# Optimization experiments

Hardware: AMD Instinct MI355X
Metric: run time of the kernel (lower is better)

## Reference

```python
import jax, jax.numpy as jnp
import numpy as np

DIM = 512; NB = 4; BS = DIM // NB            # EinFFT blocks
DS = 64; DC = 4; EXP = 2; DI = EXP * DIM      # Mamba dims
DTR = DIM // 16                               # dt_rank
BLOCKS = 2; LAM = 0.01; B_SZ = 2; L_SZ = 1024

def layer_norm(x, w, b):
    m = x.mean(-1, keepdims=True)
    v = x.var(-1, keepdims=True)
    return (x - m) / jnp.sqrt(v + 1e-5) * w + b

def softshrink(x, lam):
    return jnp.where(x > lam, x - lam, jnp.where(x < -lam, x + lam, jnp.zeros((), x.dtype)))

def mamba(x, in_proj_w, conv_w, conv_b, x_proj_w, dt_proj_w, dt_proj_b, A_log, D, out_proj_w):
    B, L, _ = x.shape
    xz = x @ in_proj_w.T                      # (B,L,2*DI)
    xm, z = jnp.split(xz, 2, axis=-1)
    # causal depthwise conv1d, keep first L outputs
    xt = xm.transpose(0, 2, 1)                # (B,DI,L)
    conv = jax.lax.conv_general_dilated(xt, conv_w, (1,), [(DC - 1, 0)],
                                        feature_group_count=DI,
                                        dimension_numbers=('NCH', 'OIH', 'NCH'))
    xm = jax.nn.silu((conv + conv_b[None, :, None]).transpose(0, 2, 1))  # (B,L,DI)
    proj = xm @ x_proj_w.T                    # (B,L,DTR+2*DS)
    dt = proj[..., :DTR]
    Bm = proj[..., DTR:DTR + DS]
    Cm = proj[..., DTR + DS:]
    dt = jax.nn.softplus(dt @ dt_proj_w.T + dt_proj_b)   # (B,L,DI)
    A = -jnp.exp(A_log)                       # (DI,DS)

    def step(h, inp):
        dt_t, B_t, C_t, u_t = inp             # (B,DI),(B,DS),(B,DS),(B,DI)
        dA = jnp.exp(dt_t[:, :, None] * A)
        h = dA * h + dt_t[:, :, None] * B_t[:, None, :] * u_t[:, :, None]
        y = jnp.einsum('bds,bs->bd', h, C_t)
        return h, y

    h0 = jnp.zeros((B, DI, DS), x.dtype)
    _, ys = jax.lax.scan(step, h0, (dt.transpose(1, 0, 2), Bm.transpose(1, 0, 2),
                                    Cm.transpose(1, 0, 2), xm.transpose(1, 0, 2)))
    y = ys.transpose(1, 0, 2) + xm * D        # (B,L,DI)
    y = y * jax.nn.silu(z)
    return y @ out_proj_w.T

def einfft(x, cw1, cw2, cb1, cb2):
    B, N, C = x.shape
    xf = jnp.fft.fft2(x.reshape(B, N, NB, BS), axes=(1, 2), norm='ortho')
    mul = lambda t, w: jnp.einsum('BNbd,bdk->BNbk', t, w)
    r1 = jax.nn.relu(mul(xf.real, cw1[0]) - mul(xf.imag, cw1[1]) + cb1[0])
    i1 = jax.nn.relu(mul(xf.real, cw1[1]) + mul(xf.imag, cw1[0]) + cb1[1])
    r2 = softshrink(mul(r1, cw2[0]) - mul(i1, cw2[1]) + cb2[0], LAM)
    i2 = softshrink(mul(r1, cw2[1]) + mul(i1, cw2[0]) + cb2[1], LAM)
    out = jnp.fft.ifft2(r2 + 1j * i2, axes=(1, 2), norm='ortho')
    return out.real.astype(x.dtype).reshape(B, N, C)

def setup_inputs() -> dict:
    key = jax.random.key(0)
    ks = jax.random.split(key, 16)
    r = lambda i, shape, s: jax.random.normal(ks[i], shape, jnp.float32) * s
    A_log = jnp.log(jnp.tile(jnp.arange(1, DS + 1, dtype=jnp.float32), (DI, 1)))
    return {
        'x': jax.random.normal(ks[0], (B_SZ, L_SZ, DIM), jnp.float32),
        'ln_w': jnp.ones((DIM,), jnp.float32), 'ln_b': jnp.zeros((DIM,), jnp.float32),
        'in_proj_w': r(1, (2 * DI, DIM), 0.02),
        'conv_w': r(2, (DI, 1, DC), 0.1), 'conv_b': jnp.zeros((DI,), jnp.float32),
        'x_proj_w': r(3, (DTR + 2 * DS, DI), 0.02),
        'dt_proj_w': r(4, (DI, DTR), 0.02),
        'dt_proj_b': jnp.full((DI,), float(np.log(np.expm1(0.01))), jnp.float32),
        'A_log': A_log, 'D': jnp.ones((DI,), jnp.float32),
        'out_proj_w': r(5, (DIM, DI), 0.02),
        'norm2_w': jnp.ones((DIM,), jnp.float32), 'norm2_b': jnp.zeros((DIM,), jnp.float32),
        'cw1': r(6, (2, NB, BS, BS), 0.02), 'cw2': r(7, (2, NB, BS, BS), 0.02),
        'cb1': r(8, (2, NB, BS), 0.02), 'cb2': r(9, (2, NB, BS), 0.02),
    }

def reference(x, ln_w, ln_b, in_proj_w, conv_w, conv_b, x_proj_w, dt_proj_w, dt_proj_b,
              A_log, D, out_proj_w, norm2_w, norm2_b, cw1, cw2, cb1, cb2):
    for _ in range(BLOCKS):
        x = x + mamba(layer_norm(x, ln_w, ln_b), in_proj_w, conv_w, conv_b,
                      x_proj_w, dt_proj_w, dt_proj_b, A_log, D, out_proj_w)
        x = x + einfft(layer_norm(x, norm2_w, norm2_b), cw1, cw2, cb1, cb2)
    return x
```

## Files before the change

### kernel.cpp

```cpp
#include <hip/hip_runtime.h>

typedef unsigned short u16;
typedef __attribute__((ext_vector_type(8))) short bf8;
typedef __attribute__((ext_vector_type(4))) float f4;

__device__ __forceinline__ float bf2f(u16 b) {
    return __uint_as_float(((unsigned)b) << 16);
}
__device__ __forceinline__ u16 f2bf(float f) {
    unsigned u = __float_as_uint(f);
    u += 0x7fffu + ((u >> 16) & 1u);
    return (u16)(u >> 16);
}
__device__ __forceinline__ void pack8f(const float* v, u16* dst) {
    uint r0 = (uint)f2bf(v[0]) | ((uint)f2bf(v[1]) << 16);
    uint r1 = (uint)f2bf(v[2]) | ((uint)f2bf(v[3]) << 16);
    uint r2 = (uint)f2bf(v[4]) | ((uint)f2bf(v[5]) << 16);
    uint r3 = (uint)f2bf(v[6]) | ((uint)f2bf(v[7]) << 16);
    *(uint4*)dst = make_uint4(r0, r1, r2, r3);
}
__device__ __forceinline__ bf8 neg8(bf8 v) {
    union { bf8 b; uint u[4]; } t; t.b = v;
    t.u[0] ^= 0x80008000u; t.u[1] ^= 0x80008000u;
    t.u[2] ^= 0x80008000u; t.u[3] ^= 0x80008000u;
// ... 21 lines not shown

struct CvtArgs {
    const void* src[18];
    void* dst[18];
    int n[18];
    int obf[18];
};
__global__ __launch_bounds__(256)
void cvt_all_k(CvtArgs a, const int* __restrict__ flag) {
    const int t = blockIdx.y;
    const int n = a.n[t];
    const int f = flag[0];
    if (a.obf[t] == 2) {
        u16* __restrict__ d = (u16*)a.dst[t];
        if (f) {
            const u16* __restrict__ s = (const u16*)a.src[t];
            for (int i = blockIdx.x * 256 + threadIdx.x; i < n; i += gridDim.x * 256) {
                int cin = i & 127, cout = (i >> 7) & 127, snb = i >> 14;
                d[(snb << 14) + (cout << 7) + cin] = s[(snb << 14) + (cin << 7) + cout];
            }
        } else {
            const float* __restrict__ s = (const float*)a.src[t];
            for (int i = blockIdx.x * 256 + threadIdx.x; i < n; i += gridDim.x * 256) {
                int cin = i & 127, cout = (i >> 7) & 127, snb = i >> 14;
                d[(snb << 14) + (cout << 7) + cin] =
                    f2bf(s[(snb << 14) + (cin << 7) + cout]);
            }
        }
    } else if (a.obf[t] == 1) {
        u16* __restrict__ d = (u16*)a.dst[t];
        if (f) {
            const u16* __restrict__ s = (const u16*)a.src[t];
            for (int i = blockIdx.x * 256 + threadIdx.x; i < n; i += gridDim.x * 256)
                d[i] = s[i];
        } else {
            const float* __restrict__ s = (const float*)a.src[t];
            for (int i = blockIdx.x * 256 + threadIdx.x; i < n; i += gridDim.x * 256)
                d[i] = f2bf(s[i]);
        }
    } else {
        float* __restrict__ d = (float*)a.dst[t];
        if (f) {
            const u16* __restrict__ s = (const u16*)a.src[t];
            for (int i = blockIdx.x * 256 + threadIdx.x; i < n; i += gridDim.x * 256)
                d[i] = bf2f(s[i]);
        } else {
            const float* __restrict__ s = (const float*)a.src[t];
            for (int i = blockIdx.x * 256 + threadIdx.x; i < n; i += gridDim.x * 256)
                d[i] = s[i];
        }
    }
}

__global__ void out_k(const float* __restrict__ in, void* __restrict__ out,
                      int n, const int* __restrict__ flag) {
    int i = blockIdx.x * 256 + threadIdx.x;
    if (i >= n) return;
    if (flag[0]) ((u16*)out)[i] = f2bf(in[i]);
    else         ((float*)out)[i] = in[i];
}

__global__ __launch_bounds__(256)
void ln_k(const float* __restrict__ x, const float* __restrict__ w,
          const float* __restrict__ b, u16* __restrict__ out) {
    const int row = blockIdx.x, tid = threadIdx.x;
    const float* xr = x + (long)row * 512;
    float v0 = xr[tid], v1 = xr[tid + 256];
    float s = v0 + v1, q = v0 * v0 + v1 * v1;
#pragma unroll
    for (int off = 32; off; off >>= 1) {
        s += __shfl_xor(s, off);
        q += __shfl_xor(q, off);
    }
    __shared__ float ss[4], qq[4];
    int wid = tid >> 6;
    if ((tid & 63) == 0) { ss[wid] = s; qq[wid] = q; }
    __syncthreads();
    s = ss[0] + ss[1] + ss[2] + ss[3];
    q = qq[0] + qq[1] + qq[2] + qq[3];
    float mean = s * (1.f / 512.f);
    float var = q * (1.f / 512.f) - mean * mean;
    float rstd = rsqrtf(var + 1e-5f);
    u16* o = out + (long)row * 512;
    o[tid]       = f2bf((v0 - mean) * rstd * w[tid]       + b[tid]);
    o[tid + 256] = f2bf((v1 - mean) * rstd * w[tid + 256] + b[tid + 256]);
}

#define LSTR 40
template <int TAF, int EPI>
__global__ __launch_bounds__(256)
void mgemm_k(const void* __restrict__ Ap, const u16* __restrict__ Bp,
             float* __restrict__ D, int N, int K, int lda, int ldb, int ldc,
             long bsA, long bsB, long bsC,
             const float* __restrict__ bias, const float* __restrict__ res) {
    const float* Af = (const float*)Ap + blockIdx.z * bsA;
    const u16*  Ab  = (const u16*)Ap + blockIdx.z * bsA;
    const u16*  B   = Bp + blockIdx.z * bsB;
    D += blockIdx.z * bsC;

    __shared__ u16 As[64 * LSTR];
    __shared__ u16 Bs[64 * LSTR];
    const int tid = threadIdx.x;
    const int lane = tid & 63;
    const int w = tid >> 6, wm = w & 1, wn = w >> 1;
    const int m0 = blockIdx.y * 64, n0 = blockIdx.x * 64;
    const int fr = (lane & 15), fq = (lane >> 4);

    f4 acc[2][2] = {};

    for (int k0 = 0; k0 < K; k0 += 32) {
        {
            const int ar = tid >> 2, aks = (tid & 3) << 3;
            if constexpr (TAF == 1) {
                *(uint4*)&As[ar * LSTR + aks] =
                    *(const uint4*)(Ab + (long)(m0 + ar) * lda + k0 + aks);
            } else if constexpr (TAF == 2) {
                const float* p = Af + (long)(m0 + ar) * lda + k0 + aks;
                float4 x = *(const float4*)p, y = *(const float4*)(p + 4);
#pragma unroll
                for (int pt = 1; pt < 4; ++pt) {
                    const float* pp = p + (long)pt * bsA;
                    float4 x1 = *(const float4*)pp, y1 = *(const float4*)(pp + 4);
                    x.x += x1.x; x.y += x1.y; x.z += x1.z; x.w += x1.w;
                    y.x += y1.x; y.y += y1.y; y.z += y1.z; y.w += y1.w;
                }
                float tv[8];
                tv[0] = x.x; tv[1] = x.y; tv[2] = x.z; tv[3] = x.w;
                tv[4] = y.x; tv[5] = y.y; tv[6] = y.z; tv[7] = y.w;
                pack8f(tv, &As[ar * LSTR + aks]);
            } else {
                const float* p = Af + (long)(m0 + ar) * lda + k0 + aks;
                float tv[8];
                float4 x = *(const float4*)p, y = *(const float4*)(p + 4);
                tv[0] = x.x; tv[1] = x.y; tv[2] = x.z; tv[3] = x.w;
                tv[4] = y.x; tv[5] = y.y; tv[6] = y.z; tv[7] = y.w;
                pack8f(tv, &As[ar * LSTR + aks]);
            }
        }
        {
            const int br = tid >> 2, bks = (tid & 3) << 3;
            uint4 raw = make_uint4(0, 0, 0, 0);
            if (n0 + br < N)
                raw = *(const uint4*)(B + (long)(n0 + br) * ldb + k0 + bks);
            *(uint4*)&Bs[br * LSTR + bks] = raw;
        }
        __syncthreads();
        bf8 af[2], bff[2];
#pragma unroll
        for (int t = 0; t < 2; t++) {
            af[t]  = *(bf8*)&As[(wm * 32 + t * 16 + fr) * LSTR + (fq << 3)];
            bff[t] = *(bf8*)&Bs[(wn * 32 + t * 16 + fr) * LSTR + (fq << 3)];
        }
#pragma unroll
        for (int i = 0; i < 2; i++)
#pragma unroll
            for (int j = 0; j < 2; j++)
                acc[i][j] = __builtin_amdgcn_mfma_f32_16x16x32_bf16(
                    af[i], bff[j], acc[i][j], 0, 0, 0);
        __syncthreads();
    }

#pragma unroll
    for (int i = 0; i < 2; i++) {
#pragma unroll
        for (int j = 0; j < 2; j++) {
            const int gmb = m0 + wm * 32 + i * 16 + (fq << 2);
            const int gn  = n0 + wn * 32 + j * 16 + fr;
            if (gn >= N) continue;
            float v[4];
#pragma unroll
            for (int e = 0; e < 4; e++) v[e] = acc[i][j][e];
            if constexpr (EPI == 1 || EPI == 3) {
                float bb = bias[gn];
#pragma unroll
                for (int e = 0; e < 4; e++) {
                    float t = v[e] + bb;
                    v[e] = (t > 20.f) ? t : log1pf(__expf(t));
                }
            }
#pragma unroll
            for (int e = 0; e < 4; e++) {
                long idx = (long)(gmb + e) * ldc + gn;
                float t = v[e];
                if constexpr (EPI == 2) t += res[idx];
                if constexpr (EPI == 3) ((u16*)D)[idx] = f2bf(t);
                else                    D[idx] = t;
            }
        }
    }
}

__global__ __launch_bounds__(256)
void gemm128_k(const u16* __restrict__ A, const u16* __restrict__ B,
               float* __restrict__ Dm, u16* __restrict__ Dz,
               int K, int lda, int ldb) {
    __shared__ u16 As[128 * LSTR];
    __shared__ u16 Bs[128 * LSTR];
    const int tid = threadIdx.x, lane = tid & 63;
    const int w = tid >> 6, wm = w & 1, wn = w >> 1;
    const int m0 = blockIdx.y * 128, n0 = blockIdx.x * 128;
    const int fr = lane & 15, fq = lane >> 4;
    f4 acc[4][4] = {};

    for (int k0 = 0; k0 < K; k0 += 32) {
#pragma unroll
        for (int j = 0; j < 2; ++j) {
            int idx = tid + j * 256;
            int row = idx >> 2, col = (idx & 3) << 3;
            *(uint4*)&As[row * LSTR + col] =
                *(const uint4*)(A + (long)(m0 + row) * lda + k0 + col);
            *(uint4*)&Bs[row * LSTR + col] =
                *(const uint4*)(B + (long)(n0 + row) * ldb + k0 + col);
        }
        __syncthreads();
        bf8 af[4], bfv[4];
#pragma unroll
        for (int i = 0; i < 4; ++i) {
            af[i]  = *(bf8*)&As[(wm * 64 + i * 16 + fr) * LSTR + (fq << 3)];
            bfv[i] = *(bf8*)&Bs[(wn * 64 + i * 16 + fr) * LSTR + (fq << 3)];
        }
#pragma unroll
        for (int i = 0; i < 4; ++i)
#pragma unroll
            for (int j = 0; j < 4; ++j)
                acc[i][j] = __builtin_amdgcn_mfma_f32_16x16x32_bf16(
                    af[i], bfv[j], acc[i][j], 0, 0, 0);
        __syncthreads();
    }
#pragma unroll
    for (int i = 0; i < 4; ++i)
#pragma unroll
        for (int j = 0; j < 4; ++j) {
            const int gm = m0 + wm * 64 + i * 16 + (fq << 2);
            const int gn = n0 + wn * 64 + j * 16 + fr;
            if (n0 < 1024) {
#pragma unroll
                for (int e = 0; e < 4; ++e)
                    Dm[(long)(gm + e) * 1024 + gn] = acc[i][j][e];
            } else {
#pragma unroll
                for (int e = 0; e < 4; ++e)
                    Dz[(long)(gm + e) * 1024 + (gn - 1024)] = f2bf(acc[i][j][e]);
            }
        }
}

__global__ __launch_bounds__(1024)
void ffw_k(const u16* __restrict__ xn, u16* __restrict__ Orb,
           u16* __restrict__ Oib) {
    const int bz = blockIdx.x;
    const int b = bz >> 7, cg = bz & 127;
    const int t = threadIdx.x;
    const int f = t >> 8, tl = t & 255;
    const int c = cg + f * 128;
    __shared__ float re[4224], im[4224], twr[768], twi[768];
    if (t < 768) {
        float s, cc;
        __sincosf((float)t * -6.1359231515425649e-3f, &s, &cc);
        twr[t] = cc; twi[t] = s;
    }
    float* rf = re + f * 1056;
    float* mf = im + f * 1056;
    const u16* src = xn + ((long)b * 1024) * 512 + c;
#pragma unroll
    for (int r = 0; r < 4; ++r) {
        int n = tl + r * 256;
        float v = bf2f(src[(long)n * 512]);
        int a = n + (n >> 5);
        rf[a] = v; mf[a] = 0.f;
    }
    __syncthreads();
#pragma unroll
    for (int st = 0; st < 5; ++st) {
        const int qsh = 8 - 2 * st;
        const int q = 1 << qsh;
        const int len = q << 2;
        const int m = 1 << (2 * st);
        int j = tl & (q - 1);
        int g = tl >> qsh;
        int i0 = g * len + j;
        int a0 = i0 + (i0 >> 5);
        int i1 = i0 + q,     a1 = i1 + (i1 >> 5);
        int i2 = i0 + 2 * q, a2 = i2 + (i2 >> 5);
        int i3 = i0 + 3 * q, a3 = i3 + (i3 >> 5);
        float ar = rf[a0], ai = mf[a0];
        float br = rf[a1], bi = mf[a1];
        float cr = rf[a2], ci = mf[a2];
        float dr = rf[a3], di = mf[a3];
        float t0r = ar + cr, t0i = ai + ci;
        float t1r = ar - cr, t1i = ai - ci;
        float t2r = br + dr, t2i = bi + di;
        float u = br - dr, v = bi - di;
        rf[a0] = t0r + t2r; mf[a0] = t0i + t2i;
        {
            int k = j * m;
            float wr = twr[k], wi = twi[k];
// ... 102 lines not shown
        const int q = 1 << qsh;
        const int len = q << 2;
        const int m = 1 << (2 * st);
        int j = tl & (q - 1);
        int g = tl >> qsh;
        int i0 = g * len + j;
        int a0 = i0 + (i0 >> 5);
        int i1 = i0 + q,     a1 = i1 + (i1 >> 5);
        int i2 = i0 + 2 * q, a2 = i2 + (i2 >> 5);
        int i3 = i0 + 3 * q, a3 = i3 + (i3 >> 5);
        float ar = rf[a0], ai = mf[a0];
        float br = rf[a1], bi = mf[a1];
        float cr = rf[a2], ci = mf[a2];
        float dr = rf[a3], di = mf[a3];
        float t0r = ar + cr, t0i = ai + ci;
        float t1r = ar - cr, t1i = ai - ci;
        float t2r = br + dr, t2i = bi + di;
        float u = br - dr, v = bi - di;
        rf[a0] = t0r + t2r; mf[a0] = t0i + t2i;
        {
            int k = j * m;
            float wr = twr[k], wi = twi[k];
            float xr = t1r - v, xi = t1i + u;
            rf[a1] = xr * wr - xi * wi;
            mf[a1] = xr * wi + xi * wr;
        }
        {
            int k = 2 * j * m;
            float wr = twr[k], wi = twi[k];
            float xr = t0r - t2r, xi = t0i - t2i;
            rf[a2] = xr * wr - xi * wi;
            mf[a2] = xr * wi + xi * wr;
        }
        {
            int k = 3 * j * m;
            float wr = twr[k], wi = twi[k];
            float xr = t1r + v, xi = t1i - u;
            rf[a3] = xr * wr - xi * wi;
            mf[a3] = xr * wi + xi * wr;
        }
        __syncthreads();
    }
    float* d = Yc + ((long)(b * 512 + c)) * 1024;
#pragma unroll
    for (int r = 0; r < 4; ++r) {
        int n = tl + r * 256;
        int sidx = digrev10(n);
        int a = sidx + (sidx >> 5);
        d[n] = rf[a] * 0.03125f;
    }
}

__global__ __launch_bounds__(256)
void transadd_k(float* __restrict__ xbuf, const float* __restrict__ Yc) {
    const int b = blockIdx.z;
    const int c0 = blockIdx.x * 64, n0 = blockIdx.y * 64;
    __shared__ float T[64][65];
    const int tid = threadIdx.x;
    const int r = tid >> 2, q = (tid & 3) * 16;
    const float* src = Yc + ((long)(b * 512 + c0 + r)) * 1024 + n0 + q;
#pragma unroll
    for (int k = 0; k < 4; ++k) {
        float4 v = *(const float4*)(src + k * 4);
        T[r][q + k * 4 + 0] = v.x; T[r][q + k * 4 + 1] = v.y;
        T[r][q + k * 4 + 2] = v.z; T[r][q + k * 4 + 3] = v.w;
    }
    __syncthreads();
    float* dst = xbuf + ((long)(b * 1024 + n0 + r)) * 512 + c0 + q;
#pragma unroll
    for (int k = 0; k < 4; ++k) {
        float4 w = *(const float4*)(dst + k * 4);
        w.x += T[q + k * 4 + 0][r]; w.y += T[q + k * 4 + 1][r];
        w.z += T[q + k * 4 + 2][r]; w.w += T[q + k * 4 + 3][r];
        *(float4*)(dst + k * 4) = w;
    }
}

#define LSTR2 136
template <int ACT>
__global__ __launch_bounds__(256)
void cmix_k(const u16* __restrict__ Xr, const u16* __restrict__ Xi,
            const u16* __restrict__ WT, const float* __restrict__ cb,
            u16* __restrict__ Or, u16* __restrict__ Oi) {
    const int z = blockIdx.z, b = z >> 2, nb = z & 3;
    const u16* Ar = Xr + (long)b * 524288 + nb * 131072;
    const u16* Ai = Xi + (long)b * 524288 + nb * 131072;
    const u16* Wr = WT + nb * 16384;
    const u16* Wi = WT + 65536 + nb * 16384;
    u16* Dr = Or + (long)b * 524288 + nb * 131072;
    u16* Di = Oi + (long)b * 524288 + nb * 131072;
    __shared__ u16 Ars[64 * LSTR2], Ais[64 * LSTR2], Brs[64 * LSTR2], Bis[64 * LSTR2];
    const int tid = threadIdx.x, lane = tid & 63;
    const int w = tid >> 6, wm = w & 1, wn = w >> 1;
    const int m0 = blockIdx.y * 64, n0 = blockIdx.x * 64;
    const int fr = (lane & 15), fq = (lane >> 4);
    f4 accr[2][2] = {}, acci[2][2] = {};

    {
        const int am = tid & 63, akb = (tid >> 6) << 3;
#pragma unroll
        for (int kk = 0; kk < 4; ++kk) {
            const int kb = kk * 32 + akb;
            u16 tr[8], ti[8];
#pragma unroll
            for (int j = 0; j < 8; j++) {
                long off = (long)(kb + j) * 1024 + m0 + am;
                tr[j] = Ar[off]; ti[j] = Ai[off];
            }
            uint r0 = (uint)tr[0] | ((uint)tr[1] << 16);
            uint r1 = (uint)tr[2] | ((uint)tr[3] << 16);
            uint r2 = (uint)tr[4] | ((uint)tr[5] << 16);
            uint r3 = (uint)tr[6] | ((uint)tr[7] << 16);
            *(uint4*)&Ars[am * LSTR2 + kb] = make_uint4(r0, r1, r2, r3);
            r0 = (uint)ti[0] | ((uint)ti[1] << 16);
            r1 = (uint)ti[2] | ((uint)ti[3] << 16);
            r2 = (uint)ti[4] | ((uint)ti[5] << 16);
            r3 = (uint)ti[6] | ((uint)ti[7] << 16);
            *(uint4*)&Ais[am * LSTR2 + kb] = make_uint4(r0, r1, r2, r3);
        }
        const int br = tid >> 2, bks = (tid & 3) << 3;
#pragma unroll
        for (int kk = 0; kk < 4; ++kk) {
            const int kb = kk * 32 + bks;
            *(uint4*)&Brs[br * LSTR2 + kb] =
                *(const uint4*)(Wr + (long)(n0 + br) * 128 + kb);
            *(uint4*)&Bis[br * LSTR2 + kb] =
                *(const uint4*)(Wi + (long)(n0 + br) * 128 + kb);
// ... 7 lines not shown
        bf8 arf[2], aif[2], brf[2], bif[2];
#pragma unroll
        for (int t = 0; t < 2; t++) {
            arf[t] = *(bf8*)&Ars[(wm * 32 + t * 16 + fr) * LSTR2 + kc];
            aif[t] = *(bf8*)&Ais[(wm * 32 + t * 16 + fr) * LSTR2 + kc];
            brf[t] = *(bf8*)&Brs[(wn * 32 + t * 16 + fr) * LSTR2 + kc];
            bif[t] = *(bf8*)&Bis[(wn * 32 + t * 16 + fr) * LSTR2 + kc];
        }
        bf8 nai[2] = { neg8(aif[0]), neg8(aif[1]) };
#pragma unroll
        for (int i = 0; i < 2; i++)
#pragma unroll
            for (int j = 0; j < 2; j++) {
                accr[i][j] = __builtin_amdgcn_mfma_f32_16x16x32_bf16(arf[i], brf[j], accr[i][j], 0, 0, 0);
                accr[i][j] = __builtin_amdgcn_mfma_f32_16x16x32_bf16(nai[i], bif[j], accr[i][j], 0, 0, 0);
                acci[i][j] = __builtin_amdgcn_mfma_f32_16x16x32_bf16(arf[i], bif[j], acci[i][j], 0, 0, 0);
                acci[i][j] = __builtin_amdgcn_mfma_f32_16x16x32_bf16(aif[i], brf[j], acci[i][j], 0, 0, 0);
            }
    }

#pragma unroll
    for (int i = 0; i < 2; i++)
#pragma unroll
        for (int j = 0; j < 2; j++) {
            const int gmb = m0 + wm * 32 + i * 16 + (fq << 2);
            const int gn  = n0 + wn * 32 + j * 16 + fr;
            const float bbr = cb[nb * 128 + gn];
            const float bbi = cb[512 + nb * 128 + gn];
            u16 pr[4], pi[4];
#pragma unroll
            for (int e = 0; e < 4; e++) {
                float vr = accr[i][j][e] + bbr;
                float vi = acci[i][j][e] + bbi;
                if (ACT == 0) {
                    vr = fmaxf(vr, 0.f);
                    vi = fmaxf(vi, 0.f);
                } else {
                    vr = (vr > 0.01f) ? vr - 0.01f : ((vr < -0.01f) ? vr + 0.01f : 0.f);
                    vi = (vi > 0.01f) ? vi - 0.01f : ((vi < -0.01f) ? vi + 0.01f : 0.f);
                }
                pr[e] = f2bf(vr); pi[e] = f2bf(vi);
            }
            uint2 wr2, wi2;
            wr2.x = (uint)pr[0] | ((uint)pr[1] << 16);
            wr2.y = (uint)pr[2] | ((uint)pr[3] << 16);
            wi2.x = (uint)pi[0] | ((uint)pi[1] << 16);
            wi2.y = (uint)pi[2] | ((uint)pi[3] << 16);
            *(uint2*)&Dr[(long)gn * 1024 + gmb] = wr2;
            *(uint2*)&Di[(long)gn * 1024 + gmb] = wi2;
        }
}

__global__ __launch_bounds__(256)
void conv_k(const float* __restrict__ xm, const float* __restrict__ cw,
            const float* __restrict__ cb, u16* __restrict__ u) {
    int idx = blockIdx.x * 256 + threadIdx.x;
    int d = idx & 1023;
    int l = (idx >> 10) & 1023;
    int b = idx >> 20;
    float acc = cb[d];
    const float* base = xm + (long)b * 1048576 + d;
#pragma unroll
    for (int j = 0; j < 4; j++) {
        int li = l - 3 + j;
        if (li >= 0) acc = fmaf(cw[d * 4 + j], base[(long)li * 1024], acc);
    }
    float sig = 1.f / (1.f + __expf(-acc));
    u[idx] = f2bf(acc * sig);
}

__global__ __launch_bounds__(256)
void scan1_k(const u16* __restrict__ dtb, const u16* __restrict__ uLb,
             const float* __restrict__ Pb, const float* __restrict__ alog,
             u16* __restrict__ Hb, float* __restrict__ Sbuf,
             float* __restrict__ Bred, float* __restrict__ Cred,
             const int* __restrict__ flag) {
    const int dg = blockIdx.x, c = blockIdx.y, b = blockIdx.z;
    const int tid = threadIdx.x;
    const int d = dg * 256 + tid;
    const int t0 = c * 16;
    __shared__ float Bls[16][64];
    {
        int r = tid >> 4, cg = (tid & 15) << 2;
        const float* src = Pb + ((long)(b * 1024 + t0 + r)) * 160 + 32 + cg;
        float4 v0 = *(const float4*)src;
        float4 v1 = *(const float4*)(src + 327680);
        float4 v2 = *(const float4*)(src + 655360);
        float4 v3 = *(const float4*)(src + 983040);
        v0.x += v1.x + v2.x + v3.x;
        v0.y += v1.y + v2.y + v3.y;
        v0.z += v1.z + v2.z + v3.z;
        v0.w += v1.w + v2.w + v3.w;
        *(float4*)&Bls[r][cg] = v0;
        if (dg == 0) {
            long ro = (((long)(b * 64 + c)) * 16 + r) * 64 + cg;
            *(float4*)&Bred[ro] = v0;
            float4 c0 = *(const float4*)(src + 64);
            float4 c1 = *(const float4*)(src + 64 + 327680);
            float4 c2 = *(const float4*)(src + 64 + 655360);
            float4 c3 = *(const float4*)(src + 64 + 983040);
            c0.x += c1.x + c2.x + c3.x;
            c0.y += c1.y + c2.y + c3.y;
            c0.z += c1.z + c2.z + c3.z;
            c0.w += c1.w + c2.w + c3.w;
            *(float4*)&Cred[ro] = c0;
        }
    }
    __syncthreads();

    float h[64];
#pragma unroll
    for (int s = 0; s < 64; s++) h[s] = 0.f;
    float S = 0.f;
    const u16* dtp = dtb + (long)(b * 1024 + t0) * 1024 + d;
    const u16* up  = uLb + (long)(b * 1024 + t0) * 1024 + d;

    if (flag[1]) {
        for (int t = 0; t < 16; ++t) {
            float dt = bf2f(dtp[(long)t * 1024]);
            float uu = bf2f(up[(long)t * 1024]);
            float dtu = dt * uu;
            S += dt;
            float q = __expf(-dt);
            float q2 = q * q, q3 = q2 * q, q4 = q2 * q2;
            float a0 = q, a1 = q2, a2 = q3, a3 = q4;
            const float4* B4p = (const float4*)&Bls[t][0];
#pragma unroll
            for (int sg = 0; sg < 16; ++sg) {
                float4 B4 = B4p[sg];
                h[sg * 4 + 0] = a0 * h[sg * 4 + 0] + dtu * B4.x;
                h[sg * 4 + 1] = a1 * h[sg * 4 + 1] + dtu * B4.y;
                h[sg * 4 + 2] = a2 * h[sg * 4 + 2] + dtu * B4.z;
                h[sg * 4 + 3] = a3 * h[sg * 4 + 3] + dtu * B4.w;
                a0 *= q4; a1 *= q4; a2 *= q4; a3 *= q4;
            }
        }
    } else {
        float A[64];
        const float* ap = alog + (long)d * 64;
#pragma unroll
        for (int s = 0; s < 64; s += 4) {
            float4 a4 = *(const float4*)(ap + s);
            A[s] = -__expf(a4.x); A[s + 1] = -__expf(a4.y);
            A[s + 2] = -__expf(a4.z); A[s + 3] = -__expf(a4.w);
        }
        for (int t = 0; t < 16; ++t) {
            float dt = bf2f(dtp[(long)t * 1024]);
            float uu = bf2f(up[(long)t * 1024]);
            float dtu = dt * uu;
            S += dt;
            const float4* B4p = (const float4*)&Bls[t][0];
#pragma unroll
            for (int sg = 0; sg < 16; ++sg) {
                float4 B4 = B4p[sg];
                h[sg * 4 + 0] = __expf(dt * A[sg * 4 + 0]) * h[sg * 4 + 0] + dtu * B4.x;
                h[sg * 4 + 1] = __expf(dt * A[sg * 4 + 1]) * h[sg * 4 + 1] + dtu * B4.y;
                h[sg * 4 + 2] = __expf(dt * A[sg * 4 + 2]) * h[sg * 4 + 2] + dtu * B4.z;
                h[sg * 4 + 3] = __expf(dt * A[sg * 4 + 3]) * h[sg * 4 + 3] + dtu * B4.w;
            }
        }
    }
    u16* Hp = Hb + ((((long)(b * 64 + c)) * 1024 + d) << 6);
#pragma unroll
    for (int s = 0; s < 64; s += 4) {
        uint2 p;
        p.x = ((__float_as_uint(h[s]) + 0x8000u) >> 16) |
              ((__float_as_uint(h[s + 1]) + 0x8000u) & 0xFFFF0000u);
        p.y = ((__float_as_uint(h[s + 2]) + 0x8000u) >> 16) |
              ((__float_as_uint(h[s + 3]) + 0x8000u) & 0xFFFF0000u);
        *(uint2*)&Hp[s] = p;
    }
    Sbuf[(b * 64 + c) * 1024 + d] = S;
}

__global__ __launch_bounds__(256)
void scan2_k(const float* __restrict__ alog, const float* __restrict__ Sbuf,
             u16* __restrict__ Hb) {
    int idx = blockIdx.x * 256 + threadIdx.x;
    int s = idx & 63, d = (idx >> 6) & 1023, b = idx >> 16;
    float A = -__expf(alog[(long)d * 64 + s]);
    float carry = 0.f;
    long off = ((((long)(b * 64)) * 1024 + d) << 6) + s;
    int sb = (b * 64) * 1024 + d;
    float Scur = Sbuf[sb];
    float Hcur = bf2f(Hb[off]);
    for (int c = 0; c < 64; ++c) {
        float Snxt = 0.f, Hnxt = 0.f;
        if (c < 63) {
            Snxt = Sbuf[sb + 1024];
            Hnxt = bf2f(Hb[off + 65536]);
        }
        float P = __expf(A * Scur);
        Hb[off] = (u16)((__float_as_uint(carry) + 0x8000u) >> 16);
        carry = P * carry + Hcur;
        Scur = Snxt; Hcur = Hnxt;
        off += 65536; sb += 1024;
    }
}

__global__ __launch_bounds__(256)
void scan3_k(const u16* __restrict__ dtb, const u16* __restrict__ uLb,
             const u16* __restrict__ zLb, const float* __restrict__ Bred,
             const float* __restrict__ Cred, const float* __restrict__ alog,
             const u16* __restrict__ Hb, const float* __restrict__ Dw,
             const int* __restrict__ flag, u16* __restrict__ y2) {
    const int dg = blockIdx.x, c = blockIdx.y, b = blockIdx.z;
    const int tid = threadIdx.x;
    const int d = dg * 256 + tid;
    const int t0 = c * 16;
    __shared__ float Bls[16][64];
    __shared__ float Cls[16][64];
    {
        int r = tid >> 4, cg = (tid & 15) << 2;
        long ro = (((long)(b * 64 + c)) * 16 + r) * 64 + cg;
        *(float4*)&Bls[r][cg] = *(const float4*)&Bred[ro];
        *(float4*)&Cls[r][cg] = *(const float4*)&Cred[ro];
    }
    __syncthreads();

    float h[64];
    const u16* Hp = Hb + ((((long)(b * 64 + c)) * 1024 + d) << 6);
#pragma unroll
    for (int s = 0; s < 64; s += 4) {
        uint2 p = *(const uint2*)&Hp[s];
        h[s]     = __uint_as_float(p.x << 16);
        h[s + 1] = __uint_as_float(p.x & 0xFFFF0000u);
        h[s + 2] = __uint_as_float(p.y << 16);
        h[s + 3] = __uint_as_float(p.y & 0xFFFF0000u);
    }
    const float Dd = Dw[d];
    const u16* dtp = dtb + (long)(b * 1024 + t0) * 1024 + d;
    const u16* up  = uLb + (long)(b * 1024 + t0) * 1024 + d;
    const u16* zp  = zLb + (long)(b * 1024 + t0) * 1024 + d;
    u16* y2p = y2 + (long)(b * 1024 + t0) * 1024 + d;

    if (flag[1]) {
        for (int t = 0; t < 16; ++t) {
            float dt = bf2f(dtp[(long)t * 1024]);
            float uu = bf2f(up[(long)t * 1024]);
            float zz = bf2f(zp[(long)t * 1024]);
            float dtu = dt * uu;
            float y = 0.f;
            float q = __expf(-dt);
            float q2 = q * q, q3 = q2 * q, q4 = q2 * q2;
            float a0 = q, a1 = q2, a2 = q3, a3 = q4;
            const float4* B4p = (const float4*)&Bls[t][0];
            const float4* C4p = (const float4*)&Cls[t][0];
#pragma unroll
            for (int sg = 0; sg < 16; ++sg) {
                float4 B4 = B4p[sg];
                float4 C4 = C4p[sg];
                h[sg * 4 + 0] = a0 * h[sg * 4 + 0] + dtu * B4.x;
                y = fmaf(h[sg * 4 + 0], C4.x, y);
                h[sg * 4 + 1] = a1 * h[sg * 4 + 1] + dtu * B4.y;
                y = fmaf(h[sg * 4 + 1], C4.y, y);
                h[sg * 4 + 2] = a2 * h[sg * 4 + 2] + dtu * B4.z;
                y = fmaf(h[sg * 4 + 2], C4.z, y);
                h[sg * 4 + 3] = a3 * h[sg * 4 + 3] + dtu * B4.w;
                y = fmaf(h[sg * 4 + 3], C4.w, y);
                a0 *= q4; a1 *= q4; a2 *= q4; a3 *= q4;
            }
            float g = zz / (1.f + __expf(-zz));
            y2p[(long)t * 1024] = f2bf((y + uu * Dd) * g);
        }
    } else {
        float A[64];
        const float* ap = alog + (long)d * 64;
#pragma unroll
        for (int s = 0; s < 64; s += 4) {
            float4 a4 = *(const float4*)(ap + s);
            A[s] = -__expf(a4.x); A[s + 1] = -__expf(a4.y);
            A[s + 2] = -__expf(a4.z); A[s + 3] = -__expf(a4.w);
        }
        for (int t = 0; t < 16; ++t) {
            float dt = bf2f(dtp[(long)t * 1024]);
            float uu = bf2f(up[(long)t * 1024]);
            float zz = bf2f(zp[(long)t * 1024]);
            float dtu = dt * uu;
            float y = 0.f;
            const float4* B4p = (const float4*)&Bls[t][0];
            const float4* C4p = (const float4*)&Cls[t][0];
#pragma unroll
            for (int sg = 0; sg < 16; ++sg) {
                float4 B4 = B4p[sg];
                float4 C4 = C4p[sg];
                h[sg * 4 + 0] = __expf(dt * A[sg * 4 + 0]) * h[sg * 4 + 0] + dtu * B4.x;
                y = fmaf(h[sg * 4 + 0], C4.x, y);
                h[sg * 4 + 1] = __expf(dt * A[sg * 4 + 1]) * h[sg * 4 + 1] + dtu * B4.y;
                y = fmaf(h[sg * 4 + 1], C4.y, y);
                h[sg * 4 + 2] = __expf(dt * A[sg * 4 + 2]) * h[sg * 4 + 2] + dtu * B4.z;
                y = fmaf(h[sg * 4 + 2], C4.z, y);
                h[sg * 4 + 3] = __expf(dt * A[sg * 4 + 3]) * h[sg * 4 + 3] + dtu * B4.w;
                y = fmaf(h[sg * 4 + 3], C4.w, y);
            }
            float g = zz / (1.f + __expf(-zz));
            y2p[(long)t * 1024] = f2bf((y + uu * Dd) * g);
        }
    }
}

extern "C" void kernel_launch(void* const* d_in, const int* in_sizes, int n_in,
                              void* d_out, int out_size, void* d_ws, size_t ws_size,
                              hipStream_t stream) {
    float* ws = (float*)d_ws;
    int* flag = (int*)ws;
    size_t o = 64;
    float* xbuf  = ws + o; o += 1048576;
    float* fftA  = ws + o; o += 3145728;
    float* xmL   = ws + o; o += 2097152;
    float* Yc    = ws + o; o += 1048576;
    u16* xnb     = (u16*)(ws + o); o += 524288;
    u16* wInpB   = (u16*)(ws + o); o += 524288;
    u16* wXpB    = (u16*)(ws + o); o += 81920;
    u16* wDtB    = (u16*)(ws + o); o += 16384;
    u16* wOutB   = (u16*)(ws + o); o += 262144;
    u16* WT1     = (u16*)(ws + o); o += 65536;
    u16* WT2     = (u16*)(ws + o); o += 65536;
    float* wConv = ws + o; o += 4096;
    float* wAlog = ws + o; o += 65536;
    float* wLnW  = ws + o; o += 512;
    float* wLnB  = ws + o; o += 512;
    float* wConvB= ws + o; o += 1024;
    float* wDtBias=ws + o; o += 1024;
    float* wD    = ws + o; o += 1024;
    float* wN2w  = ws + o; o += 512;
    float* wN2b  = ws + o; o += 512;
    float* wCb1  = ws + o; o += 1024;
    float* wCb2  = ws + o; o += 1024;
    float* Hreg  = ws + o; o += 4194304;
    float* Sbuf  = ws + o; o += 131072;
    float* Pbuf2 = ws + o; o += 1310720;
    u16* uLb     = (u16*)(ws + o); o += 1048576;
    u16* y2b     = (u16*)(ws + o); o += 524288;
    u16* dtLb    = (u16*)(ws + o); o += 1048576;
    u16* zLb     = (u16*)(ws + o); o += 1048576;
    float* Bred  = ws + o; o += 131072;
    float* Cred  = ws + o; o += 131072;
    u16* Hb    = (u16*)Hreg;
    u16* xzb  = (u16*)fftA;
    u16* Xrb  = xzb;
    u16* Xib  = xzb + 1048576;
    u16* r1b  = xzb + 2097152;
    u16* i1b  = xzb + 3145728;
    u16* X2rb = xzb + 4194304;
    u16* X2ib = xzb + 5242880;

    dim3 blk(256);

    detect_k<<<1, 1, 0, stream>>>((const u16*)d_in[8], flag);

    CvtArgs ca;
    void* dsts[18] = {xbuf, wLnW, wLnB, wInpB, wConv, wConvB, wXpB, wDtB, wDtBias,
                      wAlog, wD, wOutB, wN2w, wN2b, WT1, WT2, wCb1, wCb2};
    int obf[18]    = {0,    0,    0,    1,     0,     0,      1,    1,    0,
                      0,     0,  1,     0,    0,    2,   2,   0,    0};
    for (int i = 0; i < 18; i++) {
        ca.src[i] = d_in[i];
        ca.dst[i] = dsts[i];
        ca.n[i] = in_sizes[i];
        ca.obf[i] = obf[i];
    }
    cvt_all_k<<<dim3(64, 18), blk, 0, stream>>>(ca, flag);
    achk_k<<<256, blk, 0, stream>>>(wAlog, flag);

    for (int it = 0; it < 2; ++it) {
        ln_k<<<2048, blk, 0, stream>>>(xbuf, wLnW, wLnB, xnb);
        gemm128_k<<<dim3(16, 16), blk, 0, stream>>>(
            xnb, wInpB, xmL, zLb, 512, 512, 512);
        conv_k<<<8192, blk, 0, stream>>>(xmL, wConv, wConvB, uLb);
        mgemm_k<1, 0><<<dim3(3, 32, 4), blk, 0, stream>>>(
            uLb, wXpB, Pbuf2, 160, 256, 1024, 1024, 160,
            256, 256, 327680, nullptr, nullptr);
        mgemm_k<2, 3><<<dim3(16, 32, 1), blk, 0, stream>>>(
            Pbuf2, wDtB, (float*)dtLb, 1024, 32, 160, 32, 1024, 327680, 0, 0,
            wDtBias, nullptr);
        scan1_k<<<dim3(4, 64, 2), blk, 0, stream>>>(
            dtLb, uLb, Pbuf2, wAlog, Hb, Sbuf, Bred, Cred, flag);
        scan2_k<<<512, blk, 0, stream>>>(wAlog, Sbuf, Hb);
        scan3_k<<<dim3(4, 64, 2), blk, 0, stream>>>(
            dtLb, uLb, zLb, Bred, Cred, wAlog, Hb, wD, flag, y2b);
        mgemm_k<1, 2><<<dim3(8, 32, 1), blk, 0, stream>>>(
            y2b, wOutB, xbuf, 512, 1024, 1024, 1024, 512, 0, 0, 0, nullptr, xbuf);

        ln_k<<<2048, blk, 0, stream>>>(xbuf, wN2w, wN2b, xnb);
        ffw_k<<<256, dim3(1024), 0, stream>>>(xnb, Xrb, Xib);
        cmix_k<0><<<dim3(2, 16, 8), blk, 0, stream>>>(Xrb, Xib, WT1, wCb1, r1b, i1b);
        cmix_k<1><<<dim3(2, 16, 8), blk, 0, stream>>>(r1b, i1b, WT2, wCb2, X2rb, X2ib);
        ifw_k<<<256, dim3(1024), 0, stream>>>(X2rb, X2ib, Yc);
        transadd_k<<<dim3(8, 16, 2), blk, 0, stream>>>(xbuf, Yc);
    }

    out_k<<<(out_size + 255) / 256, blk, 0, stream>>>(xbuf, d_out, out_size, flag);
}
```

Measured before the change: 461.6 us.

## Fuse dt projection into scan1, enlarge scan chunks, store xm as bf16

The dt_proj GEMM with softplus is folded into scan1_k, which now computes dt per channel from shared-memory x_proj rows and writes the bf16 dt for scan3. The scan chunk length doubles from 16 to 32 timesteps, which halves the number of chunks and the work of the carry pass in scan2. The in_proj output for xm is stored as bf16 instead of fp32 to cut conv input traffic. The final output conversion is fused into the last transadd. Risks: fewer blocks in scan1 and scan3, higher register use with 32-entry arrays under launch_bounds(256,1), and reduced precision for xm.

```diff
diff --git a/kernel.cpp b/kernel.cpp
--- a/kernel.cpp
+++ b/kernel.cpp
@@ -97,14 +97,6 @@
     }
 }
 
-__global__ void out_k(const float* __restrict__ in, void* __restrict__ out,
-                      int n, const int* __restrict__ flag) {
-    int i = blockIdx.x * 256 + threadIdx.x;
-    if (i >= n) return;
-    if (flag[0]) ((u16*)out)[i] = f2bf(in[i]);
-    else         ((float*)out)[i] = in[i];
-}
-
 __global__ __launch_bounds__(256)
 void ln_k(const float* __restrict__ x, const float* __restrict__ w,
           const float* __restrict__ b, u16* __restrict__ out) {
@@ -159,20 +151,6 @@
             if constexpr (TAF == 1) {
                 *(uint4*)&As[ar * LSTR + aks] =
                     *(const uint4*)(Ab + (long)(m0 + ar) * lda + k0 + aks);
-            } else if constexpr (TAF == 2) {
-                const float* p = Af + (long)(m0 + ar) * lda + k0 + aks;
-                float4 x = *(const float4*)p, y = *(const float4*)(p + 4);
-#pragma unroll
-                for (int pt = 1; pt < 4; ++pt) {
-                    const float* pp = p + (long)pt * bsA;
-                    float4 x1 = *(const float4*)pp, y1 = *(const float4*)(pp + 4);
-                    x.x += x1.x; x.y += x1.y; x.z += x1.z; x.w += x1.w;
-                    y.x += y1.x; y.y += y1.y; y.z += y1.z; y.w += y1.w;
-                }
-                float tv[8];
-                tv[0] = x.x; tv[1] = x.y; tv[2] = x.z; tv[3] = x.w;
-                tv[4] = y.x; tv[5] = y.y; tv[6] = y.z; tv[7] = y.w;
-                pack8f(tv, &As[ar * LSTR + aks]);
             } else {
                 const float* p = Af + (long)(m0 + ar) * lda + k0 + aks;
                 float tv[8];
@@ -212,24 +190,12 @@
             const int gmb = m0 + wm * 32 + i * 16 + (fq << 2);
             const int gn  = n0 + wn * 32 + j * 16 + fr;
             if (gn >= N) continue;
-            float v[4];
-#pragma unroll
-            for (int e = 0; e < 4; e++) v[e] = acc[i][j][e];
-            if constexpr (EPI == 1 || EPI == 3) {
-                float bb = bias[gn];
-#pragma unroll
-                for (int e = 0; e < 4; e++) {
-                    float t = v[e] + bb;
-                    v[e] = (t > 20.f) ? t : log1pf(__expf(t));
-                }
-            }
 #pragma unroll
             for (int e = 0; e < 4; e++) {
                 long idx = (long)(gmb + e) * ldc + gn;
-                float t = v[e];
+                float t = acc[i][j][e];
                 if constexpr (EPI == 2) t += res[idx];
-                if constexpr (EPI == 3) ((u16*)D)[idx] = f2bf(t);
-                else                    D[idx] = t;
+                D[idx] = t;
             }
         }
     }
@@ -237,7 +203,7 @@
 
 __global__ __launch_bounds__(256)
 void gemm128_k(const u16* __restrict__ A, const u16* __restrict__ B,
-               float* __restrict__ Dm, u16* __restrict__ Dz,
+               u16* __restrict__ Dm, u16* __restrict__ Dz,
                int K, int lda, int ldb) {
     __shared__ u16 As[128 * LSTR];
     __shared__ u16 Bs[128 * LSTR];
@@ -272,21 +238,17 @@
                     af[i], bfv[j], acc[i][j], 0, 0, 0);
         __syncthreads();
     }
+    u16* Dst = (n0 < 1024) ? Dm : Dz;
+    const int noff = (n0 < 1024) ? 0 : 1024;
 #pragma unroll
     for (int i = 0; i < 4; ++i)
 #pragma unroll
         for (int j = 0; j < 4; ++j) {
             const int gm = m0 + wm * 64 + i * 16 + (fq << 2);
-            const int gn = n0 + wn * 64 + j * 16 + fr;
-            if (n0 < 1024) {
-#pragma unroll
-                for (int e = 0; e < 4; ++e)
-                    Dm[(long)(gm + e) * 1024 + gn] = acc[i][j][e];
-            } else {
-#pragma unroll
-                for (int e = 0; e < 4; ++e)
-                    Dz[(long)(gm + e) * 1024 + (gn - 1024)] = f2bf(acc[i][j][e]);
-            }
+            const int gn = n0 + wn * 64 + j * 16 + fr - noff;
+#pragma unroll
+            for (int e = 0; e < 4; ++e)
+                Dst[(long)(gm + e) * 1024 + gn] = f2bf(acc[i][j][e]);
         }
 }
 
@@ -495,7 +457,8 @@
 }
 
 __global__ __launch_bounds__(256)
-void transadd_k(float* __restrict__ xbuf, const float* __restrict__ Yc) {
+void transadd_k(float* __restrict__ xbuf, const float* __restrict__ Yc,
+                void* __restrict__ dout, int last, const int* __restrict__ flag) {
     const int b = blockIdx.z;
     const int c0 = blockIdx.x * 64, n0 = blockIdx.y * 64;
     __shared__ float T[64][65];
@@ -509,13 +472,32 @@
         T[r][q + k * 4 + 2] = v.z; T[r][q + k * 4 + 3] = v.w;
     }
     __syncthreads();
-    float* dst = xbuf + ((long)(b * 1024 + n0 + r)) * 512 + c0 + q;
-#pragma unroll
-    for (int k = 0; k < 4; ++k) {
-        float4 w = *(const float4*)(dst + k * 4);
-        w.x += T[q + k * 4 + 0][r]; w.y += T[q + k * 4 + 1][r];
-        w.z += T[q + k * 4 + 2][r]; w.w += T[q + k * 4 + 3][r];
-        *(float4*)(dst + k * 4) = w;
+    const long base = ((long)(b * 1024 + n0 + r)) * 512 + c0 + q;
+    float* dst = xbuf + base;
+    if (last) {
+        const int bf = flag[0];
+#pragma unroll
+        for (int k = 0; k < 4; ++k) {
+            float4 w = *(const float4*)(dst + k * 4);
+            w.x += T[q + k * 4 + 0][r]; w.y += T[q + k * 4 + 1][r];
+            w.z += T[q + k * 4 + 2][r]; w.w += T[q + k * 4 + 3][r];
+            if (bf) {
+                uint2 p;
+                p.x = (uint)f2bf(w.x) | ((uint)f2bf(w.y) << 16);
+                p.y = (uint)f2bf(w.z) | ((uint)f2bf(w.w) << 16);
+                *(uint2*)((u16*)dout + base + k * 4) = p;
+            } else {
+                *(float4*)((float*)dout + base + k * 4) = w;
+            }
+        }
+    } else {
+#pragma unroll
+        for (int k = 0; k < 4; ++k) {
+            float4 w = *(const float4*)(dst + k * 4);
+            w.x += T[q + k * 4 + 0][r]; w.y += T[q + k * 4 + 1][r];
+            w.z += T[q + k * 4 + 2][r]; w.w += T[q + k * 4 + 3][r];
+            *(float4*)(dst + k * 4) = w;
+        }
     }
 }
 
@@ -629,74 +611,134 @@
 }
 
 __global__ __launch_bounds__(256)
-void conv_k(const float* __restrict__ xm, const float* __restrict__ cw,
+void conv_k(const u16* __restrict__ xm, const float* __restrict__ cw,
             const float* __restrict__ cb, u16* __restrict__ u) {
     int idx = blockIdx.x * 256 + threadIdx.x;
     int d = idx & 1023;
     int l = (idx >> 10) & 1023;
     int b = idx >> 20;
     float acc = cb[d];
-    const float* base = xm + (long)b * 1048576 + d;
+    const u16* base = xm + (long)b * 1048576 + d;
 #pragma unroll
     for (int j = 0; j < 4; j++) {
         int li = l - 3 + j;
-        if (li >= 0) acc = fmaf(cw[d * 4 + j], base[(long)li * 1024], acc);
+        if (li >= 0) acc = fmaf(cw[d * 4 + j], bf2f(base[(long)li * 1024]), acc);
     }
     float sig = 1.f / (1.f + __expf(-acc));
     u[idx] = f2bf(acc * sig);
 }
 
-__global__ __launch_bounds__(256)
-void scan1_k(const u16* __restrict__ dtb, const u16* __restrict__ uLb,
-             const float* __restrict__ Pb, const float* __restrict__ alog,
-             u16* __restrict__ Hb, float* __restrict__ Sbuf,
-             float* __restrict__ Bred, float* __restrict__ Cred,
+__global__ __launch_bounds__(256, 1)
+void scan1_k(const u16* __restrict__ uLb, const float* __restrict__ Pb,
+             const u16* __restrict__ dtW, const float* __restrict__ dtBias,
+             const float* __restrict__ alog, u16* __restrict__ Hb,
+             float* __restrict__ Sbuf, float* __restrict__ Bred,
+             float* __restrict__ Cred, u16* __restrict__ dtLb,
              const int* __restrict__ flag) {
     const int dg = blockIdx.x, c = blockIdx.y, b = blockIdx.z;
     const int tid = threadIdx.x;
     const int d = dg * 256 + tid;
-    const int t0 = c * 16;
-    __shared__ float Bls[16][64];
+    const int t0 = c * 32;
+    __shared__ float Bls[32][64];
+    __shared__ float Pls[32][32];
     {
-        int r = tid >> 4, cg = (tid & 15) << 2;
-        const float* src = Pb + ((long)(b * 1024 + t0 + r)) * 160 + 32 + cg;
-        float4 v0 = *(const float4*)src;
-        float4 v1 = *(const float4*)(src + 327680);
-        float4 v2 = *(const float4*)(src + 655360);
-        float4 v3 = *(const float4*)(src + 983040);
-        v0.x += v1.x + v2.x + v3.x;
-        v0.y += v1.y + v2.y + v3.y;
-        v0.z += v1.z + v2.z + v3.z;
-        v0.w += v1.w + v2.w + v3.w;
-        *(float4*)&Bls[r][cg] = v0;
+#pragma unroll
+        for (int j = 0; j < 2; ++j) {
+            int slot = tid + j * 256;
+            int r = slot >> 4, cg = (slot & 15) << 2;
+            const float* src = Pb + ((long)(b * 1024 + t0 + r)) * 160 + 32 + cg;
+            float4 v0 = *(const float4*)src;
+            float4 v1 = *(const float4*)(src + 327680);
+            float4 v2 = *(const float4*)(src + 655360);
+            float4 v3 = *(const float4*)(src + 983040);
+            v0.x += v1.x + v2.x + v3.x;
+            v0.y += v1.y + v2.y + v3.y;
+            v0.z += v1.z + v2.z + v3.z;
+            v0.w += v1.w + v2.w + v3.w;
+            *(float4*)&Bls[r][cg] = v0;
+            if (dg == 0)
+                *(float4*)&Bred[(((long)(b * 1024 + t0 + r)) << 6) + cg] = v0;
+        }
+        {
+            int r = tid >> 3, cg = (tid & 7) << 2;
+            const float* src = Pb + ((long)(b * 1024 + t0 + r)) * 160 + cg;
+            float4 v0 = *(const float4*)src;
+            float4 v1 = *(const float4*)(src + 327680);
+            float4 v2 = *(const float4*)(src + 655360);
+            float4 v3 = *(const float4*)(src + 983040);
+            v0.x += v1.x + v2.x + v3.x;
+            v0.y += v1.y + v2.y + v3.y;
+            v0.z += v1.z + v2.z + v3.z;
+            v0.w += v1.w + v2.w + v3.w;
+            *(float4*)&Pls[r][cg] = v0;
+        }
         if (dg == 0) {
-            long ro = (((long)(b * 64 + c)) * 16 + r) * 64 + cg;
-            *(float4*)&Bred[ro] = v0;
-            float4 c0 = *(const float4*)(src + 64);
-            float4 c1 = *(const float4*)(src + 64 + 327680);
-            float4 c2 = *(const float4*)(src + 64 + 655360);
-            float4 c3 = *(const float4*)(src + 64 + 983040);
-            c0.x += c1.x + c2.x + c3.x;
-            c0.y += c1.y + c2.y + c3.y;
-            c0.z += c1.z + c2.z + c3.z;
-            c0.w += c1.w + c2.w + c3.w;
-            *(float4*)&Cred[ro] = c0;
+#pragma unroll
+            for (int j = 0; j < 2; ++j) {
+                int slot = tid + j * 256;
+                int r = slot >> 4, cg = (slot & 15) << 2;
+                const float* src = Pb + ((long)(b * 1024 + t0 + r)) * 160 + 96 + cg;
+                float4 v0 = *(const float4*)src;
+                float4 v1 = *(const float4*)(src + 327680);
+                float4 v2 = *(const float4*)(src + 655360);
+                float4 v3 = *(const float4*)(src + 983040);
+                v0.x += v1.x + v2.x + v3.x;
+                v0.y += v1.y + v2.y + v3.y;
+                v0.z += v1.z + v2.z + v3.z;
+                v0.w += v1.w + v2.w + v3.w;
+                *(float4*)&Cred[(((long)(b * 1024 + t0 + r)) << 6) + cg] = v0;
+            }
         }
     }
     __syncthreads();
+
+    float w[32];
+    {
+        const u16* wr = dtW + (long)d * 32;
+#pragma unroll
+        for (int qi = 0; qi < 4; ++qi) {
+            uint4 qv = *((const uint4*)wr + qi);
+            w[qi * 8 + 0] = bf2f((u16)(qv.x & 0xFFFF));
+            w[qi * 8 + 1] = bf2f((u16)(qv.x >> 16));
+            w[qi * 8 + 2] = bf2f((u16)(qv.y & 0xFFFF));
+            w[qi * 8 + 3] = bf2f((u16)(qv.y >> 16));
+            w[qi * 8 + 4] = bf2f((u16)(qv.z & 0xFFFF));
+            w[qi * 8 + 5] = bf2f((u16)(qv.z >> 16));
+            w[qi * 8 + 6] = bf2f((u16)(qv.w & 0xFFFF));
+            w[qi * 8 + 7] = bf2f((u16)(qv.w >> 16));
+        }
+    }
+    const float bias = dtBias[d];
+
+    const u16* up = uLb + (long)(b * 1024 + t0) * 1024 + d;
+    float uu[32];
+#pragma unroll
+    for (int t = 0; t < 32; ++t) uu[t] = bf2f(up[(long)t * 1024]);
+    u16* dtp = dtLb + (long)(b * 1024 + t0) * 1024 + d;
 
     float h[64];
 #pragma unroll
     for (int s = 0; s < 64; s++) h[s] = 0.f;
     float S = 0.f;
-    const u16* dtp = dtb + (long)(b * 1024 + t0) * 1024 + d;
-    const u16* up  = uLb + (long)(b * 1024 + t0) * 1024 + d;
 
     if (flag[1]) {
-        for (int t = 0; t < 16; ++t) {
-            float dt = bf2f(dtp[(long)t * 1024]);
-            float uu = bf2f(up[(long)t * 1024]);
-            float dtu = dt * uu;
+        for (int t = 0; t < 32; ++t) {
+            const float4* P4 = (const float4*)&Pls[t][0];
+            float x0 = bias, x1 = 0.f, x2 = 0.f, x3 = 0.f;
+#pragma unroll
+            for (int kg = 0; kg < 8; ++kg) {
+                float4 p = P4[kg];
+                x0 = fmaf(p.x, w[kg * 4 + 0], x0);
+                x1 = fmaf(p.y, w[kg * 4 + 1], x1);
+                x2 = fmaf(p.z, w[kg * 4 + 2], x2);
+                x3 = fmaf(p.w, w[kg * 4 + 3], x3);
+            }
+            float x = (x0 + x1) + (x2 + x3);
+            float dtf = (x > 20.f) ? x : log1pf(__expf(x));
+            u16 dq = f2bf(dtf);
+            dtp[(long)t * 1024] = dq;
+            float dt = bf2f(dq);
+            float dtu = dt * uu[t];
             S += dt;
             float q = __expf(-dt);
             float q2 = q * q, q3 = q2 * q, q4 = q2 * q2;
@@ -721,10 +763,23 @@
             A[s] = -__expf(a4.x); A[s + 1] = -__expf(a4.y);
             A[s + 2] = -__expf(a4.z); A[s + 3] = -__expf(a4.w);
         }
-        for (int t = 0; t < 16; ++t) {
-            float dt = bf2f(dtp[(long)t * 1024]);
-            float uu = bf2f(up[(long)t * 1024]);
-            float dtu = dt * uu;
+        for (int t = 0; t < 32; ++t) {
+            const float4* P4 = (const float4*)&Pls[t][0];
+            float x0 = bias, x1 = 0.f, x2 = 0.f, x3 = 0.f;
+#pragma unroll
+            for (int kg = 0; kg < 8; ++kg) {
+                float4 p = P4[kg];
+                x0 = fmaf(p.x, w[kg * 4 + 0], x0);
+                x1 = fmaf(p.y, w[kg * 4 + 1], x1);
+                x2 = fmaf(p.z, w[kg * 4 + 2], x2);
+                x3 = fmaf(p.w, w[kg * 4 + 3], x3);
+            }
+            float x = (x0 + x1) + (x2 + x3);
+            float dtf = (x > 20.f) ? x : log1pf(__expf(x));
+            u16 dq = f2bf(dtf);
+            dtp[(long)t * 1024] = dq;
+            float dt = bf2f(dq);
+            float dtu = dt * uu[t];
             S += dt;
             const float4* B4p = (const float4*)&Bls[t][0];
 #pragma unroll
@@ -737,7 +792,7 @@
             }
         }
     }
-    u16* Hp = Hb + ((((long)(b * 64 + c)) * 1024 + d) << 6);
+    u16* Hp = Hb + ((((long)(b * 32 + c)) * 1024 + d) << 6);
 #pragma unroll
     for (int s = 0; s < 64; s += 4) {
         uint2 p;
@@ -747,7 +802,7 @@
               ((__float_as_uint(h[s + 3]) + 0x8000u) & 0xFFFF0000u);
         *(uint2*)&Hp[s] = p;
     }
-    Sbuf[(b * 64 + c) * 1024 + d] = S;
+    Sbuf[(b * 32 + c) * 1024 + d] = S;
 }
 
 __global__ __launch_bounds__(256)
@@ -757,13 +812,13 @@
     int s = idx & 63, d = (idx >> 6) & 1023, b = idx >> 16;
     float A = -__expf(alog[(long)d * 64 + s]);
     float carry = 0.f;
-    long off = ((((long)(b * 64)) * 1024 + d) << 6) + s;
-    int sb = (b * 64) * 1024 + d;
+    long off = (((long)(b * 32) * 1024 + d) << 6) + s;
+    int sb = (b * 32) * 1024 + d;
     float Scur = Sbuf[sb];
     float Hcur = bf2f(Hb[off]);
-    for (int c = 0; c < 64; ++c) {
+    for (int c = 0; c < 32; ++c) {
         float Snxt = 0.f, Hnxt = 0.f;
-        if (c < 63) {
+        if (c < 31) {
             Snxt = Sbuf[sb + 1024];
             Hnxt = bf2f(Hb[off + 65536]);
         }
@@ -775,7 +830,7 @@
     }
 }
 
-__global__ __launch_bounds__(256)
+__global__ __launch_bounds__(256, 1)
 void scan3_k(const u16* __restrict__ dtb, const u16* __restrict__ uLb,
              const u16* __restrict__ zLb, const float* __restrict__ Bred,
              const float* __restrict__ Cred, const float* __restrict__ alog,
@@ -784,19 +839,23 @@
     const int dg = blockIdx.x, c = blockIdx.y, b = blockIdx.z;
     const int tid = threadIdx.x;
     const int d = dg * 256 + tid;
-    const int t0 = c * 16;
-    __shared__ float Bls[16][64];
-    __shared__ float Cls[16][64];
+    const int t0 = c * 32;
+    __shared__ float Bls[32][64];
+    __shared__ float Cls[32][64];
     {
-        int r = tid >> 4, cg = (tid & 15) << 2;
-        long ro = (((long)(b * 64 + c)) * 16 + r) * 64 + cg;
-        *(float4*)&Bls[r][cg] = *(const float4*)&Bred[ro];
-        *(float4*)&Cls[r][cg] = *(const float4*)&Cred[ro];
+#pragma unroll
+        for (int j = 0; j < 2; ++j) {
+            int slot = tid + j * 256;
+            int r = slot >> 4, cg = (slot & 15) << 2;
+            long ro = (((long)(b * 1024 + t0 + r)) << 6) + cg;
+            *(float4*)&Bls[r][cg] = *(const float4*)&Bred[ro];
+            *(float4*)&Cls[r][cg] = *(const float4*)&Cred[ro];
+        }
     }
     __syncthreads();
 
     float h[64];
-    const u16* Hp = Hb + ((((long)(b * 64 + c)) * 1024 + d) << 6);
+    const u16* Hp = Hb + ((((long)(b * 32 + c)) * 1024 + d) << 6);
 #pragma unroll
     for (int s = 0; s < 64; s += 4) {
         uint2 p = *(const uint2*)&Hp[s];
@@ -811,12 +870,18 @@
     const u16* zp  = zLb + (long)(b * 1024 + t0) * 1024 + d;
     u16* y2p = y2 + (long)(b * 1024 + t0) * 1024 + d;
 
+    float uu[32], dtv[32];
+#pragma unroll
+    for (int t = 0; t < 32; ++t) {
+        uu[t]  = bf2f(up[(long)t * 1024]);
+        dtv[t] = bf2f(dtp[(long)t * 1024]);
+    }
+
     if (flag[1]) {
-        for (int t = 0; t < 16; ++t) {
-            float dt = bf2f(dtp[(long)t * 1024]);
-            float uu = bf2f(up[(long)t * 1024]);
+        for (int t = 0; t < 32; ++t) {
             float zz = bf2f(zp[(long)t * 1024]);
-            float dtu = dt * uu;
+            float dt = dtv[t];
+            float dtu = dt * uu[t];
             float y = 0.f;
             float q = __expf(-dt);
             float q2 = q * q, q3 = q2 * q, q4 = q2 * q2;
@@ -838,7 +903,7 @@
                 a0 *= q4; a1 *= q4; a2 *= q4; a3 *= q4;
             }
             float g = zz / (1.f + __expf(-zz));
-            y2p[(long)t * 1024] = f2bf((y + uu * Dd) * g);
+            y2p[(long)t * 1024] = f2bf((y + uu[t] * Dd) * g);
         }
     } else {
         float A[64];
@@ -849,11 +914,10 @@
             A[s] = -__expf(a4.x); A[s + 1] = -__expf(a4.y);
             A[s + 2] = -__expf(a4.z); A[s + 3] = -__expf(a4.w);
         }
-        for (int t = 0; t < 16; ++t) {
-            float dt = bf2f(dtp[(long)t * 1024]);
-            float uu = bf2f(up[(long)t * 1024]);
+        for (int t = 0; t < 32; ++t) {
             float zz = bf2f(zp[(long)t * 1024]);
-            float dtu = dt * uu;
+            float dt = dtv[t];
+            float dtu = dt * uu[t];
             float y = 0.f;
             const float4* B4p = (const float4*)&Bls[t][0];
             const float4* C4p = (const float4*)&Cls[t][0];
@@ -871,7 +935,7 @@
                 y = fmaf(h[sg * 4 + 3], C4.w, y);
             }
             float g = zz / (1.f + __expf(-zz));
-            y2p[(long)t * 1024] = f2bf((y + uu * Dd) * g);
+            y2p[(long)t * 1024] = f2bf((y + uu[t] * Dd) * g);
         }
     }
 }
@@ -884,7 +948,7 @@
     size_t o = 64;
     float* xbuf  = ws + o; o += 1048576;
     float* fftA  = ws + o; o += 3145728;
-    float* xmL   = ws + o; o += 2097152;
+    u16* xmb     = (u16*)(ws + o); o += 1048576;
     float* Yc    = ws + o; o += 1048576;
     u16* xnb     = (u16*)(ws + o); o += 524288;
     u16* wInpB   = (u16*)(ws + o); o += 524288;
@@ -908,7 +972,7 @@
     float* Sbuf  = ws + o; o += 131072;
     float* Pbuf2 = ws + o; o += 1310720;
     u16* uLb     = (u16*)(ws + o); o += 1048576;
-    u16* y2b     = (u16*)(ws + o); o += 524288;
+    u16* y2b     = (u16*)(ws + o); o += 1048576;
     u16* dtLb    = (u16*)(ws + o); o += 1048576;
     u16* zLb     = (u16*)(ws + o); o += 1048576;
     float* Bred  = ws + o; o += 131072;
@@ -943,18 +1007,15 @@
     for (int it = 0; it < 2; ++it) {
         ln_k<<<2048, blk, 0, stream>>>(xbuf, wLnW, wLnB, xnb);
         gemm128_k<<<dim3(16, 16), blk, 0, stream>>>(
-            xnb, wInpB, xmL, zLb, 512, 512, 512);
-        conv_k<<<8192, blk, 0, stream>>>(xmL, wConv, wConvB, uLb);
+            xnb, wInpB, xmb, zLb, 512, 512, 512);
+        conv_k<<<8192, blk, 0, stream>>>(xmb, wConv, wConvB, uLb);
         mgemm_k<1, 0><<<dim3(3, 32, 4), blk, 0, stream>>>(
             uLb, wXpB, Pbuf2, 160, 256, 1024, 1024, 160,
             256, 256, 327680, nullptr, nullptr);
-        mgemm_k<2, 3><<<dim3(16, 32, 1), blk, 0, stream>>>(
-            Pbuf2, wDtB, (float*)dtLb, 1024, 32, 160, 32, 1024, 327680, 0, 0,
-            wDtBias, nullptr);
-        scan1_k<<<dim3(4, 64, 2), blk, 0, stream>>>(
-            dtLb, uLb, Pbuf2, wAlog, Hb, Sbuf, Bred, Cred, flag);
+        scan1_k<<<dim3(4, 32, 2), blk, 0, stream>>>(
+            uLb, Pbuf2, wDtB, wDtBias, wAlog, Hb, Sbuf, Bred, Cred, dtLb, flag);
         scan2_k<<<512, blk, 0, stream>>>(wAlog, Sbuf, Hb);
-        scan3_k<<<dim3(4, 64, 2), blk, 0, stream>>>(
+        scan3_k<<<dim3(4, 32, 2), blk, 0, stream>>>(
             dtLb, uLb, zLb, Bred, Cred, wAlog, Hb, wD, flag, y2b);
         mgemm_k<1, 2><<<dim3(8, 32, 1), blk, 0, stream>>>(
             y2b, wOutB, xbuf, 512, 1024, 1024, 1024, 512, 0, 0, 0, nullptr, xbuf);
@@ -964,8 +1025,6 @@
         cmix_k<0><<<dim3(2, 16, 8), blk, 0, stream>>>(Xrb, Xib, WT1, wCb1, r1b, i1b);
         cmix_k<1><<<dim3(2, 16, 8), blk, 0, stream>>>(r1b, i1b, WT2, wCb2, X2rb, X2ib);
         ifw_k<<<256, dim3(1024), 0, stream>>>(X2rb, X2ib, Yc);
-        transadd_k<<<dim3(8, 16, 2), blk, 0, stream>>>(xbuf, Yc);
-    }
-
-    out_k<<<(out_size + 255) / 256, blk, 0, stream>>>(xbuf, d_out, out_size, flag);
-}
+        transadd_k<<<dim3(8, 16, 2), blk, 0, stream>>>(xbuf, Yc, d_out, it == 1, flag);
+    }
+}
```

New measurement: 445.1 us. 1.04x faster.
